# Kernel optimization log

Measured on AMD Instinct MI355X. Metric: run time of the kernel, lower is better.

The kernel has to match this reference:

```python
import jax, jax.numpy as jnp
import numpy as np
from jax import lax

T_STEPS = 1024
BATCH = 1024
NUM_STATES = 64


def setup_inputs() -> dict:
    key = jax.random.key(0)
    k_em, k_len, k_start, k_stop, k_trans = jax.random.split(key, 5)
    emission_factors = jax.random.normal(k_em, (T_STEPS, BATCH, NUM_STATES), dtype=jnp.float32)
    sequence_sizes = jax.random.randint(k_len, (BATCH,), 1, T_STEPS + 1, dtype=jnp.int32)
    start_factors = jax.random.normal(k_start, (NUM_STATES,), dtype=jnp.float32)
    stop_factors = jax.random.normal(k_stop, (NUM_STATES,), dtype=jnp.float32)
    transition_factors = jax.random.normal(k_trans, (NUM_STATES, NUM_STATES), dtype=jnp.float32)
    return {
        "emission_factors": emission_factors,
        "sequence_sizes": sequence_sizes,
        "start_factors": start_factors,
        "stop_factors": stop_factors,
        "transition_factors": transition_factors,
    }


def reference(emission_factors, sequence_sizes, start_factors, stop_factors, transition_factors):
    # emission_factors: [T, B, S] time-major; sequence_sizes: [B] lengths in [1, T].
    # Linear-chain CRF forward algorithm (log-partition):
    #   alpha_0   = start + em_0
    #   alpha_t[s] = logsumexp_p(alpha_{t-1}[p] + trans[s, p]) + em_t[s]   (while active)
    #   log_Z     = logsumexp_s(alpha_{L-1}[s] + stop[s])
    # Masked scan: alpha is frozen once a sequence ends, matching the packed
    # variable-batch-size iteration of the original (penultimate_alphas).
    max_steps = emission_factors.shape[0]

    alpha0 = start_factors[None, :] + emission_factors[0]  # [B, S]
    # active[t-1, b] = (t < length_b) for t = 1..T-1
    active = (jnp.arange(1, max_steps)[:, None] < sequence_sizes[None, :])[:, :, None]  # [T-1, B, 1]

    def step(alpha, inp):
        em_t, act = inp  # em_t: [B, S], act: [B, 1]
        # alpha[b, None, p] + trans[None, s, p] -> logsumexp over p
        new_alpha = jax.nn.logsumexp(alpha[:, None, :] + transition_factors[None, :, :], axis=2) + em_t
        return jnp.where(act, new_alpha, alpha), None

    alpha, _ = lax.scan(step, alpha0, (emission_factors[1:], active))
    log_normalizer = jax.nn.logsumexp(alpha + stop_factors[None, :], axis=1)  # [B]
    return log_normalizer
```

## Files before the change

### kernel.cpp

```cpp
#include <hip/hip_runtime.h>

#define T_STEPS 1024
#define BATCH   1024
#define NS      64
#define CPB     16
#define NBLK    (BATCH / CPB)
#define TS      ((size_t)BATCH * NS)

typedef __attribute__((ext_vector_type(8))) __bf16 bf16x8;
typedef __attribute__((ext_vector_type(4))) float  f32x4;

#define SWZ_XOR16 0x401F
__device__ __forceinline__ float swz16f(float x) {
    return __uint_as_float((unsigned)__builtin_amdgcn_ds_swizzle(
        (int)__float_as_uint(x), SWZ_XOR16));
}

__global__ __launch_bounds__(64)
void crf_fwd_v11(const float* __restrict__ em,
                 const int*   __restrict__ seqlen,
                 const float* __restrict__ start,
                 const float* __restrict__ stop,
                 const float* __restrict__ trans,
                 float*       __restrict__ out) {
    const int l  = threadIdx.x;
    const int c  = l & 15;
    const int g  = l >> 4;
    const int b0 = blockIdx.x * CPB;
    const int Lc = seqlen[b0 + c];

    bf16x8 ae[4][2];
#pragma unroll
    for (int mt = 0; mt < 4; ++mt)
#pragma unroll
        for (int ks = 0; ks < 2; ++ks) {
            const float* rp = trans + (size_t)(16 * mt + c) * NS + 32 * ks + 4 * g;
            f32x4 t0 = *(const f32x4*)rp;
            f32x4 t1 = *(const f32x4*)(rp + 16);
            bf16x8 a;
            a[0] = (__bf16)__expf(t0[0]); a[1] = (__bf16)__expf(t0[1]);
            a[2] = (__bf16)__expf(t0[2]); a[3] = (__bf16)__expf(t0[3]);
            a[4] = (__bf16)__expf(t1[0]); a[5] = (__bf16)__expf(t1[1]);
            a[6] = (__bf16)__expf(t1[2]); a[7] = (__bf16)__expf(t1[3]);
            ae[mt][ks] = a;
        }

    float es[4][4];
#pragma unroll
    for (int mt = 0; mt < 4; ++mt) {
        f32x4 sv = *(const f32x4*)(stop + 16 * mt + 4 * g);
#pragma unroll
        for (int i = 0; i < 4; ++i) es[mt][i] = __expf(sv[i]);
    }

    const float* emp = em + (size_t)(b0 + c) * NS + 4 * g;

    f32x4 emb[4][4];
    float u[4][4];
    f32x4 acc[4];
    bf16x8 bfA, bfB;
    float mloc, cacc, inv;

#define CAPT(T_)                                                              \
    do {                                                                      \
        float dv_ = 0.f;                                                      \
        _Pragma("unroll") for (int m_ = 0; m_ < 4; ++m_)                      \
            _Pragma("unroll") for (int i_ = 0; i_ < 4; ++i_)                  \
                dv_ = fmaf(u[m_][i_], es[m_][i_], dv_);                       \
        dv_ += swz16f(dv_);                                                   \
        dv_ += __shfl_xor(dv_, 32, 64);                                       \
        if ((T_) == Lc - 1 && g == 0) out[b0 + c] = __logf(dv_) + cacc;       \
    } while (0)

#define PACKB()                                                               \
    do {                                                                      \
        bf16x8 xa_, xb_;                                                      \
        xa_[0] = (__bf16)u[0][0]; xa_[1] = (__bf16)u[0][1];                   \
        xa_[2] = (__bf16)u[0][2]; xa_[3] = (__bf16)u[0][3];                   \
        xa_[4] = (__bf16)u[1][0]; xa_[5] = (__bf16)u[1][1];                   \
        xa_[6] = (__bf16)u[1][2]; xa_[7] = (__bf16)u[1][3];                   \
        xb_[0] = (__bf16)u[2][0]; xb_[1] = (__bf16)u[2][1];                   \
        xb_[2] = (__bf16)u[2][2]; xb_[3] = (__bf16)u[2][3];                   \
        xb_[4] = (__bf16)u[3][0]; xb_[5] = (__bf16)u[3][1];                   \
        xb_[6] = (__bf16)u[3][2]; xb_[7] = (__bf16)u[3][3];                   \
        bfA = xa_; bfB = xb_;                                                 \
    } while (0)

#define STEP(T_, SLOT_, RN_, LAST_)                                           \
    do {                                                                      \
        f32x4 zz_ = {0.f, 0.f, 0.f, 0.f};                                     \
        _Pragma("unroll") for (int m_ = 0; m_ < 4; ++m_)                      \
            acc[m_] = __builtin_amdgcn_mfma_f32_16x16x32_bf16(                \
                ae[m_][0], bfA, zz_, 0, 0, 0);                                \
        _Pragma("unroll") for (int m_ = 0; m_ < 4; ++m_)                      \
            acc[m_] = __builtin_amdgcn_mfma_f32_16x16x32_bf16(                \
                ae[m_][1], bfB, acc[m_], 0, 0, 0);                            \
        if (RN_) {                                                            \
            float v1_ = fmaxf(mloc, swz16f(mloc));                            \
            float mm_ = fmaxf(v1_, __shfl_xor(v1_, 32, 64));                  \
            mm_ = fmaxf(mm_, 1e-30f);                                         \
            inv = __builtin_amdgcn_rcpf(mm_);                                 \
            cacc += __logf(mm_);                                              \
        }                                                                     \
        _Pragma("unroll") for (int m_ = 0; m_ < 4; ++m_)                      \
            _Pragma("unroll") for (int i_ = 0; i_ < 4; ++i_) {                \
                float exv_ = __expf(emb[SLOT_][m_][i_]);                      \
                if (RN_) exv_ *= inv;                                         \
                u[m_][i_] = acc[m_][i_] * exv_;                               \
            }                                                                 \
        {            \
            size_t tn_ = (size_t)(((T_) + 4 <= T_STEPS - 1) ? (T_) + 4        \
                                                            : T_STEPS - 1);   \
            const float* p_ = emp + tn_ * TS;                                 \
            _Pragma("unroll") for (int m_ = 0; m_ < 4; ++m_)                  \
                emb[SLOT_][m_] = *(const f32x4*)(p_ + 16 * m_);               \
        }                                                                     \
        if (__any((T_) == Lc - 1)) CAPT(T_);                                  \
        if (LAST_) {                                                          \
            mloc = u[0][0];                                                   \
            _Pragma("unroll") for (int m_ = 0; m_ < 4; ++m_)                  \
                _Pragma("unroll") for (int i_ = 0; i_ < 4; ++i_)              \
                    mloc = fmaxf(mloc, u[m_][i_]);                            \
        }                                                                     \
        PACKB();                                                              \
    } while (0)

#pragma unroll
    for (int S = 0; S < 4; ++S)
#pragma unroll
        for (int mt = 0; mt < 4; ++mt)
            emb[S][mt] = *(const f32x4*)(emp + (size_t)S * TS + 16 * mt);
#pragma unroll
    for (int mt = 0; mt < 4; ++mt) {
        f32x4 sv = *(const f32x4*)(start + 16 * mt + 4 * g);
#pragma unroll
        for (int i = 0; i < 4; ++i)
            u[mt][i] = __expf(sv[i] + emb[0][mt][i]);
    }
#pragma unroll
    for (int mt = 0; mt < 4; ++mt)
        emb[0][mt] = *(const f32x4*)(emp + (size_t)4 * TS + 16 * mt);

    cacc = 0.f; inv = 1.f; (void)inv;
    if (__any(0 == Lc - 1)) CAPT(0);

    mloc = u[0][0];
#pragma unroll
    for (int mt = 0; mt < 4; ++mt)
#pragma unroll
        for (int i = 0; i < 4; ++i) mloc = fmaxf(mloc, u[mt][i]);

    PACKB();

    for (int grp = 0; grp < 256; ++grp) {
        const int t0_ = 1 + 4 * grp;
        STEP(t0_ + 0, 1, 1, 0);
        STEP(t0_ + 1, 2, 0, 0);
        STEP(t0_ + 2, 3, 0, 0);
        STEP(t0_ + 3, 0, 0, 1);
    }
}

extern "C" void kernel_launch(void* const* d_in, const int* in_sizes, int n_in,
                              void* d_out, int out_size, void* d_ws, size_t ws_size,
                              hipStream_t stream) {
    const float* em     = (const float*)d_in[0];
    const int*   seqlen = (const int*)  d_in[1];
    const float* start  = (const float*)d_in[2];
    const float* stop   = (const float*)d_in[3];
    const float* trans  = (const float*)d_in[4];
    float*       out    = (float*)d_out;

    crf_fwd_v11<<<NBLK, 64, 0, stream>>>(em, seqlen, start, stop, trans, out);
}
```

Before: 527.4 us.

## Split CRF scan into compute and producer waves with LDS exp staging and early exit

```diff
diff --git a/kernel.cpp b/kernel.cpp
--- a/kernel.cpp
+++ b/kernel.cpp
@@ -16,50 +16,43 @@
         (int)__float_as_uint(x), SWZ_XOR16));
 }
 
-__global__ __launch_bounds__(64)
-void crf_fwd_v11(const float* __restrict__ em,
+#define BARRIER() asm volatile("s_barrier" ::: "memory")
+#define LGKM0()   asm volatile("s_waitcnt lgkmcnt(0)" ::: "memory")
+
+__global__ __launch_bounds__(128)
+void crf_fwd_v12(const float* __restrict__ em,
                  const int*   __restrict__ seqlen,
                  const float* __restrict__ start,
                  const float* __restrict__ stop,
                  const float* __restrict__ trans,
                  float*       __restrict__ out) {
-    const int l  = threadIdx.x;
-    const int c  = l & 15;
-    const int g  = l >> 4;
-    const int b0 = blockIdx.x * CPB;
-    const int Lc = seqlen[b0 + c];
+    __shared__ f32x4 exb[4][4][4][64];
+
+    const int tid = threadIdx.x;
+    const int wv  = tid >> 6;
+    const int l   = tid & 63;
+    const int c   = l & 15;
+    const int g   = l >> 4;
+    const int b0  = blockIdx.x * CPB;
+    const int Lc  = seqlen[b0 + c];
+
+    int tmax = Lc;
+#pragma unroll
+    for (int o = 1; o < 16; o <<= 1) {
+        int t_ = __shfl_xor(tmax, o, 64);
+        tmax = tmax > t_ ? tmax : t_;
+    }
+    const int NGRP = (tmax + 2) >> 2;
+
+    const float* emB = em + (size_t)(b0 + c) * NS + 4 * g;
 
     bf16x8 ae[4][2];
-#pragma unroll
-    for (int mt = 0; mt < 4; ++mt)
-#pragma unroll
-        for (int ks = 0; ks < 2; ++ks) {
-            const float* rp = trans + (size_t)(16 * mt + c) * NS + 32 * ks + 4 * g;
-            f32x4 t0 = *(const f32x4*)rp;
-            f32x4 t1 = *(const f32x4*)(rp + 16);
-            bf16x8 a;
-            a[0] = (__bf16)__expf(t0[0]); a[1] = (__bf16)__expf(t0[1]);
-            a[2] = (__bf16)__expf(t0[2]); a[3] = (__bf16)__expf(t0[3]);
-            a[4] = (__bf16)__expf(t1[0]); a[5] = (__bf16)__expf(t1[1]);
-            a[6] = (__bf16)__expf(t1[2]); a[7] = (__bf16)__expf(t1[3]);
-            ae[mt][ks] = a;
-        }
-
-    float es[4][4];
-#pragma unroll
-    for (int mt = 0; mt < 4; ++mt) {
-        f32x4 sv = *(const f32x4*)(stop + 16 * mt + 4 * g);
-#pragma unroll
-        for (int i = 0; i < 4; ++i) es[mt][i] = __expf(sv[i]);
-    }
-
-    const float* emp = em + (size_t)(b0 + c) * NS + 4 * g;
-
-    f32x4 emb[4][4];
-    float u[4][4];
-    f32x4 acc[4];
+    float  es[4][4];
+    float  u[4][4];
+    f32x4  acc[4];
     bf16x8 bfA, bfB;
-    float mloc, cacc, inv;
+    float  mloc = 0.f, cacc = 0.f, inv = 1.f;
+    f32x4 rawE[4][4], rawO[4][4];
 
 #define CAPT(T_)                                                              \
     do {                                                                      \
@@ -86,8 +79,12 @@
         bfA = xa_; bfB = xb_;                                                 \
     } while (0)
 
-#define STEP(T_, SLOT_, RN_, LAST_)                                           \
-    do {                                                                      \
+#define CSTEP(G_, J_, RN_, LAST_)                                             \
+    do {                                                                      \
+        const int t_ = 4 * (G_) + 1 + (J_);                                   \
+        f32x4 exq[4];                                                         \
+        _Pragma("unroll") for (int m_ = 0; m_ < 4; ++m_)                      \
+            exq[m_] = exb[(G_) & 3][J_][m_][l];                               \
         f32x4 zz_ = {0.f, 0.f, 0.f, 0.f};                                     \
         _Pragma("unroll") for (int m_ = 0; m_ < 4; ++m_)                      \
             acc[m_] = __builtin_amdgcn_mfma_f32_16x16x32_bf16(                \
@@ -104,18 +101,11 @@
         }                                                                     \
         _Pragma("unroll") for (int m_ = 0; m_ < 4; ++m_)                      \
             _Pragma("unroll") for (int i_ = 0; i_ < 4; ++i_) {                \
-                float exv_ = __expf(emb[SLOT_][m_][i_]);                      \
+                float exv_ = exq[m_][i_];                                     \
                 if (RN_) exv_ *= inv;                                         \
                 u[m_][i_] = acc[m_][i_] * exv_;                               \
             }                                                                 \
-        {            \
-            size_t tn_ = (size_t)(((T_) + 4 <= T_STEPS - 1) ? (T_) + 4        \
-                                                            : T_STEPS - 1);   \
-            const float* p_ = emp + tn_ * TS;                                 \
-            _Pragma("unroll") for (int m_ = 0; m_ < 4; ++m_)                  \
-                emb[SLOT_][m_] = *(const f32x4*)(p_ + 16 * m_);               \
-        }                                                                     \
-        if (__any((T_) == Lc - 1)) CAPT(T_);                                  \
+        if (__any(t_ == Lc - 1)) CAPT(t_);                                    \
         if (LAST_) {                                                          \
             mloc = u[0][0];                                                   \
             _Pragma("unroll") for (int m_ = 0; m_ < 4; ++m_)                  \
@@ -125,39 +115,121 @@
         PACKB();                                                              \
     } while (0)
 
-#pragma unroll
-    for (int S = 0; S < 4; ++S)
+#define CGRP(G_)                                                              \
+    do {                                                                      \
+        CSTEP(G_, 0, 1, 0);                                                   \
+        CSTEP(G_, 1, 0, 0);                                                   \
+        CSTEP(G_, 2, 0, 0);                                                   \
+        CSTEP(G_, 3, 0, 1);                                                   \
+    } while (0)
+
+#define PHALF(W_, RAW_, L_)                                                   \
+    do {                                                                      \
+        const int bw_ = (W_) & 3;                                             \
+        _Pragma("unroll") for (int j_ = 0; j_ < 4; ++j_)                      \
+            _Pragma("unroll") for (int m_ = 0; m_ < 4; ++m_) {                \
+                f32x4 r_ = RAW_[j_][m_], x_;                                  \
+                x_[0] = __expf(r_[0]); x_[1] = __expf(r_[1]);                 \
+                x_[2] = __expf(r_[2]); x_[3] = __expf(r_[3]);                 \
+                exb[bw_][j_][m_][l] = x_;                                     \
+            }                                                                 \
+        _Pragma("unroll") for (int j_ = 0; j_ < 4; ++j_) {                    \
+            int tl_ = 4 * (L_) + 1 + j_;                                      \
+            if (tl_ > T_STEPS - 1) tl_ = T_STEPS - 1;                         \
+            _Pragma("unroll") for (int m_ = 0; m_ < 4; ++m_)                  \
+                RAW_[j_][m_] =                                                \
+                    *(const f32x4*)(emB + (size_t)tl_ * TS + 16 * m_);        \
+        }                                                                     \
+    } while (0)
+
+    if (wv == 0) {
 #pragma unroll
         for (int mt = 0; mt < 4; ++mt)
-            emb[S][mt] = *(const f32x4*)(emp + (size_t)S * TS + 16 * mt);
-#pragma unroll
-    for (int mt = 0; mt < 4; ++mt) {
-        f32x4 sv = *(const f32x4*)(start + 16 * mt + 4 * g);
-#pragma unroll
-        for (int i = 0; i < 4; ++i)
-            u[mt][i] = __expf(sv[i] + emb[0][mt][i]);
+#pragma unroll
+            for (int ks = 0; ks < 2; ++ks) {
+                const float* rp =
+                    trans + (size_t)(16 * mt + c) * NS + 32 * ks + 4 * g;
+                f32x4 t0 = *(const f32x4*)rp;
+                f32x4 t1 = *(const f32x4*)(rp + 16);
+                bf16x8 a;
+                a[0] = (__bf16)__expf(t0[0]); a[1] = (__bf16)__expf(t0[1]);
+                a[2] = (__bf16)__expf(t0[2]); a[3] = (__bf16)__expf(t0[3]);
+                a[4] = (__bf16)__expf(t1[0]); a[5] = (__bf16)__expf(t1[1]);
+                a[6] = (__bf16)__expf(t1[2]); a[7] = (__bf16)__expf(t1[3]);
+                ae[mt][ks] = a;
+            }
+#pragma unroll
+        for (int mt = 0; mt < 4; ++mt) {
+            f32x4 sv = *(const f32x4*)(stop + 16 * mt + 4 * g);
+#pragma unroll
+            for (int i = 0; i < 4; ++i) es[mt][i] = __expf(sv[i]);
+        }
+#pragma unroll
+        for (int mt = 0; mt < 4; ++mt) {
+            f32x4 e0 = *(const f32x4*)(emB + 16 * mt);
+            f32x4 sv = *(const f32x4*)(start + 16 * mt + 4 * g);
+#pragma unroll
+            for (int i = 0; i < 4; ++i)
+                u[mt][i] = __expf(sv[i] + e0[i]);
+        }
+        cacc = 0.f; inv = 1.f; (void)inv;
+        if (__any(0 == Lc - 1)) CAPT(0);
+        mloc = u[0][0];
+#pragma unroll
+        for (int mt = 0; mt < 4; ++mt)
+#pragma unroll
+            for (int i = 0; i < 4; ++i) mloc = fmaxf(mloc, u[mt][i]);
+        PACKB();
+    } else {
+#pragma unroll
+        for (int W = 0; W < 2; ++W) {
+            f32x4 tmp[4][4];
+#pragma unroll
+            for (int j = 0; j < 4; ++j) {
+                int t = 4 * W + 1 + j;
+                if (t > T_STEPS - 1) t = T_STEPS - 1;
+#pragma unroll
+                for (int mt = 0; mt < 4; ++mt)
+                    tmp[j][mt] = *(const f32x4*)(emB + (size_t)t * TS + 16 * mt);
+            }
+#pragma unroll
+            for (int j = 0; j < 4; ++j)
+#pragma unroll
+                for (int mt = 0; mt < 4; ++mt) {
+                    f32x4 r = tmp[j][mt], x;
+                    x[0] = __expf(r[0]); x[1] = __expf(r[1]);
+                    x[2] = __expf(r[2]); x[3] = __expf(r[3]);
+                    exb[W][j][mt][l] = x;
+                }
+        }
+#pragma unroll
+        for (int j = 0; j < 4; ++j) {
+            int t2 = 4 * 2 + 1 + j; if (t2 > T_STEPS - 1) t2 = T_STEPS - 1;
+            int t3 = 4 * 3 + 1 + j; if (t3 > T_STEPS - 1) t3 = T_STEPS - 1;
+#pragma unroll
+            for (int mt = 0; mt < 4; ++mt) {
+                rawE[j][mt] = *(const f32x4*)(emB + (size_t)t2 * TS + 16 * mt);
+                rawO[j][mt] = *(const f32x4*)(emB + (size_t)t3 * TS + 16 * mt);
+            }
+        }
+        LGKM0();
     }
-#pragma unroll
-    for (int mt = 0; mt < 4; ++mt)
-        emb[0][mt] = *(const f32x4*)(emp + (size_t)4 * TS + 16 * mt);
-
-    cacc = 0.f; inv = 1.f; (void)inv;
-    if (__any(0 == Lc - 1)) CAPT(0);
-
-    mloc = u[0][0];
-#pragma unroll
-    for (int mt = 0; mt < 4; ++mt)
-#pragma unroll
-        for (int i = 0; i < 4; ++i) mloc = fmaxf(mloc, u[mt][i]);
-
-    PACKB();
-
-    for (int grp = 0; grp < 256; ++grp) {
-        const int t0_ = 1 + 4 * grp;
-        STEP(t0_ + 0, 1, 1, 0);
-        STEP(t0_ + 1, 2, 0, 0);
-        STEP(t0_ + 2, 3, 0, 0);
-        STEP(t0_ + 3, 0, 0, 1);
+
+    for (int G = 0; G < NGRP; G += 2) {
+        BARRIER();
+        if (wv == 0) {
+            CGRP(G);
+        } else {
+            PHALF(G + 2, rawE, G + 4);
+            LGKM0();
+        }
+        BARRIER();
+        if (wv == 0) {
+            CGRP(G + 1);
+        } else {
+            PHALF(G + 3, rawO, G + 5);
+            LGKM0();
+        }
     }
 }
 
@@ -171,5 +243,5 @@
     const float* trans  = (const float*)d_in[4];
     float*       out    = (float*)d_out;
 
-    crf_fwd_v11<<<NBLK, 64, 0, stream>>>(em, seqlen, start, stop, trans, out);
+    crf_fwd_v12<<<NBLK, 128, 0, stream>>>(em, seqlen, start, stop, trans, out);
 }
```

After: 632.9 us. 20.0% more time.
